# Performance work log

Hardware: AMD Instinct MI355X
Metric: run time of the kernel (lower is better)

## Reference

```python
import jax, jax.numpy as jnp
import numpy as np

NUM_EXPERTS = 64
TOP_K = 2
NOISE_STD = 1.0
LOAD_BALANCE_WEIGHT = 0.01
NOISE_KEY = jax.random.fold_in(jax.random.key(0), 12345)


def setup_inputs() -> dict:
    key = jax.random.key(0)
    k1, k2, k3 = jax.random.split(key, 3)
    B, S, D = 4, 4096, 1024
    x = jax.random.normal(k1, (B, S, D), dtype=jnp.float32)
    W_gate = jax.random.normal(k2, (NUM_EXPERTS, D), dtype=jnp.float32) * (1.0 / np.sqrt(D))
    W_noise = jax.random.normal(k3, (NUM_EXPERTS, D), dtype=jnp.float32) * (1.0 / np.sqrt(D))
    return {"x": x, "W_gate": W_gate, "W_noise": W_noise}


def reference(x, W_gate, W_noise):
    # x: [B,S,D], W_gate/W_noise: [E,D] (torch Linear weight layout)
    clean_logits = jnp.einsum("bsd,ed->bse", x, W_gate)           # [B,S,E]
    noise_scale = jax.nn.softplus(jnp.einsum("bsd,ed->bse", x, W_noise))
    noise = jax.random.normal(NOISE_KEY, clean_logits.shape, clean_logits.dtype)
    logits = clean_logits + noise * noise_scale * NOISE_STD

    probs = jax.nn.softmax(logits, axis=-1)                        # [B,S,E]
    routing_weights, expert_indices = jax.lax.top_k(probs, TOP_K)  # [B,S,K]
    routing_weights = routing_weights / jnp.sum(routing_weights, axis=-1, keepdims=True)

    # Load-balance loss on clean logits
    B, S, E = clean_logits.shape
    num_tokens = B * S
    expert_mask = jax.nn.one_hot(expert_indices, E, dtype=jnp.float32).sum(axis=2)  # [B,S,E]
    tokens_per_expert = expert_mask.sum(axis=(0, 1))               # [E]
    fraction_tokens = tokens_per_expert / num_tokens
    router_probs = jax.nn.softmax(clean_logits, axis=-1)
    mean_router_prob = router_probs.mean(axis=(0, 1))              # [E]
    load_balance_loss = LOAD_BALANCE_WEIGHT * E * jnp.sum(fraction_tokens * mean_router_prob)

    noise_scale_mean = noise_scale.mean()
    return (routing_weights, expert_indices, load_balance_loss, router_probs, noise_scale_mean)
```

## Files before the change

### kernel.cpp

```cpp
#include <hip/hip_runtime.h>
#include <stdint.h>

#define TOKENS 16384
#define DDIM   1024
#define NEXP   64
#define NCOL   128
#define TB     32
#define NBLK   (TOKENS / TB)
#define NCH    (DDIM / 32)
#define NTILE  8
#define CPP    4

typedef __attribute__((ext_vector_type(8))) short bf16x8;
typedef __attribute__((ext_vector_type(4))) float f32x4;

__device__ ushort g_wf[3][NTILE][NCH][64][8];
__device__ float g_ps[NEXP];
__device__ float g_cnt[NEXP];
__device__ float g_spa[1];

__device__ inline ushort bf16rne(float f) {
  uint32_t u = __float_as_uint(f);
  return (ushort)((u + 0x7fffu + ((u >> 16) & 1u)) >> 16);
}
__device__ inline float bf16tof(ushort h) {
  return __uint_as_float(((uint32_t)h) << 16);
}
__device__ inline void split3(float v, ushort& h, ushort& m, ushort& l) {
  h = bf16rne(v);
  float r1 = v - bf16tof(h);
  m = bf16rne(r1);
  float r2 = r1 - bf16tof(m);
  l = bf16rne(r2);
}

struct U2 { uint32_t a, b; };

__host__ __device__ constexpr U2 tf2x32(uint32_t k0, uint32_t k1,
                                        uint32_t x0, uint32_t x1) {
  uint32_t ks[3] = {k0, k1, k0 ^ k1 ^ 0x1BD11BDAu};
  const uint32_t rot[2][4] = {{13u, 15u, 26u, 6u}, {17u, 29u, 16u, 24u}};
  x0 += ks[0]; x1 += ks[1];
  for (int d = 0; d < 5; ++d) {
    for (int j = 0; j < 4; ++j) {
      uint32_t r = rot[d & 1][j];
      x0 += x1;
      x1 = (x1 << r) | (x1 >> (32u - r));
      x1 ^= x0;
    }
    x0 += ks[(d + 1) % 3];
    x1 += ks[(d + 2) % 3] + (uint32_t)(d + 1);
  }
  return U2{x0, x1};
}

__device__ inline uint32_t noise_bits(uint32_t i) {
  constexpr U2 NK = tf2x32(0u, 0u, 0u, 12345u);
  U2 o = tf2x32(NK.a, NK.b, 0u, i);
  return o.a ^ o.b;
}

__device__ inline float xla_erfinv(float x) {
  float w = -log1pf(-x * x);
  float p;
  if (w < 5.0f) {
    w = w - 2.5f;
    p = 2.81022636e-08f;
    p = 3.43273939e-07f + p * w;
    p = -3.5233877e-06f + p * w;
    p = -4.39150654e-06f + p * w;
    p = 0.00021858087f + p * w;
    p = -0.00125372503f + p * w;
    p = -0.00417768164f + p * w;
    p = 0.246640727f + p * w;
    p = 1.50140941f + p * w;
  } else {
    w = sqrtf(w) - 3.0f;
    p = -0.000200214257f;
    p = 0.000100950558f + p * w;
    p = 0.00134934322f + p * w;
    p = -0.00367342844f + p * w;
    p = 0.00573950773f + p * w;
    p = -0.0076224613f + p * w;
    p = 0.00943887047f + p * w;
    p = 1.00167406f + p * w;
    p = 2.83297682f + p * w;
  }
  return p * x;
}

__device__ inline float noise_normal(uint32_t i) {
  uint32_t bits = noise_bits(i);
  float f = __uint_as_float((bits >> 9) | 0x3f800000u) - 1.0f;
  float u = f * 2.0f + (-0.99999994f);
  u = fmaxf(u, -0.99999994f);
  return 1.41421356237f * xla_erfinv(u);
}

__device__ inline float softplus_ref(float x) {
  return fmaxf(x, 0.0f) + log1pf(expf(-fabsf(x)));
}

__device__ inline float wave_max64(float v) {
  #pragma unroll
  for (int off = 32; off; off >>= 1) v = fmaxf(v, __shfl_xor(v, off, 64));
  return v;
}
__device__ inline float wave_sum64(float v) {
  #pragma unroll
  for (int off = 32; off; off >>= 1) v += __shfl_xor(v, off, 64);
  return v;
}
__device__ inline void wave_argmax64(float v, int idx, float& mv, int& mi) {
  float bv = v; int bi = idx;
  #pragma unroll
  for (int off = 32; off; off >>= 1) {
    float ov = __shfl_xor(bv, off, 64);
    int   oi = __shfl_xor(bi, off, 64);
    if (ov > bv || (ov == bv && oi < bi)) { bv = ov; bi = oi; }
  }
  mv = bv; mi = bi;
}

__global__ __launch_bounds__(64)
void wsplit_kernel(const float* __restrict__ wg, const float* __restrict__ wn) {
  const int ct   = blockIdx.x >> 5;
  const int kc   = blockIdx.x & 31;
  const int lane = threadIdx.x;
  const int col  = ct * 16 + (lane & 15);
  const int koff = kc * 32 + (lane >> 4) * 8;
  const float* src = (col < NEXP) ? (wg + (size_t)col * DDIM)
                                  : (wn + (size_t)(col - NEXP) * DDIM);
  const float4 v0 = *(const float4*)&src[koff];
  const float4 v1 = *(const float4*)&src[koff + 4];
  const float av[8] = {v0.x, v0.y, v0.z, v0.w, v1.x, v1.y, v1.z, v1.w};
  union BF8 { bf16x8 v; ushort u[8]; };
  BF8 H, M, L;
  #pragma unroll
  for (int j = 0; j < 8; ++j) {
    ushort h, m, l;
    split3(av[j], h, m, l);
    H.u[j] = h; M.u[j] = m; L.u[j] = l;
  }
  *(bf16x8*)&g_wf[0][ct][kc][lane][0] = H.v;
  *(bf16x8*)&g_wf[1][ct][kc][lane][0] = M.v;
  *(bf16x8*)&g_wf[2][ct][kc][lane][0] = L.v;

  if (blockIdx.x == 0) {
    g_ps[lane] = 0.0f; g_cnt[lane] = 0.0f;
    if (lane == 0) g_spa[0] = 0.0f;
  }
}

__global__ __launch_bounds__(512, 8)
void NoisyTopKRouter_57621281243491_kernel(
    const float* __restrict__ x, float* __restrict__ out) {
  __shared__ ushort ldsA[3][2][CPP][64][8];

  const int tid  = threadIdx.x;
  const int w    = tid >> 6;
  const int lane = tid & 63;
  const int tok0 = blockIdx.x * TB;

  char* LA = (char*)&ldsA[0][0][0][0][0];

  const int srow = tid >> 4;
  const int skq  = tid & 15;
  const int stg  = srow >> 4;
  const int sfr  = srow & 15;
  const int sc   = skq >> 2;
  const int ss   = skq & 3;
  const int so   = (sc * 1024 + ss * 256 + sfr * 16) ^ ((skq & 7) << 4);
  const float* sx = x + (size_t)(tok0 + srow) * DDIM + skq * 8;

  const int fr_row = lane & 15;
  const int fr_s   = lane >> 4;
  const ushort* wf = &g_wf[0][0][0][0][0];
  const int b0 = w * 16384 + lane * 8;
  #define PS 131072

  f32x4 acc0 = {0.f, 0.f, 0.f, 0.f};
  f32x4 acc1 = {0.f, 0.f, 0.f, 0.f};

  float4 xa0, xa1, xb0, xb1;

  #define SPLIT_PHASE(X0, X1)                                             \
    {                                                                     \
      union BF8 { bf16x8 v; ushort u[8]; };                               \
      BF8 H, M, L;                                                        \
      const float av_[8] = {X0.x, X0.y, X0.z, X0.w, X1.x, X1.y, X1.z, X1.w}; \
      _Pragma("unroll")                                                   \
      for (int j = 0; j < 8; ++j) {                                       \
        ushort h_, m_, l_;                                                \
        split3(av_[j], h_, m_, l_);                                       \
        H.u[j] = h_; M.u[j] = m_; L.u[j] = l_;                            \
      }                                                                   \
      *(bf16x8*)(LA + stg * 4096 + so)         = H.v;                     \
      *(bf16x8*)(LA + 8192 + stg * 4096 + so)  = M.v;                     \
      *(bf16x8*)(LA + 16384 + stg * 4096 + so) = L.v;                     \
    }

  #define MFMA_PHASE(ph)                                                  \
    _Pragma("unroll")                                                     \
    for (int c = 0; c < CPP; ++c) {                                       \
      int ro = c * 1024 + lane * 16;                                      \
      ro ^= ((ro >> 8) & 7) << 4;                                         \
      const bf16x8 Ah0 = *(const bf16x8*)(LA + ro);                       \
      const bf16x8 Am0 = *(const bf16x8*)(LA + 8192 + ro);                \
      const bf16x8 Al0 = *(const bf16x8*)(LA + 16384 + ro);               \
      const bf16x8 Ah1 = *(const bf16x8*)(LA + 4096 + ro);                \
      const bf16x8 Am1 = *(const bf16x8*)(LA + 12288 + ro);               \
      const bf16x8 Al1 = *(const bf16x8*)(LA + 20480 + ro);               \
      const int co = ((ph) * CPP + c) * 512;                              \
      const bf16x8 Bh = *(const bf16x8*)&wf[b0 + co];                     \
      const bf16x8 Bm = *(const bf16x8*)&wf[b0 + PS + co];                \
      const bf16x8 Bl = *(const bf16x8*)&wf[b0 + 2 * PS + co];            \
      acc0 = __builtin_amdgcn_mfma_f32_16x16x32_bf16(Ah0, Bh, acc0, 0, 0, 0); \
      acc0 = __builtin_amdgcn_mfma_f32_16x16x32_bf16(Ah0, Bm, acc0, 0, 0, 0); \
      acc0 = __builtin_amdgcn_mfma_f32_16x16x32_bf16(Am0, Bh, acc0, 0, 0, 0); \
      acc0 = __builtin_amdgcn_mfma_f32_16x16x32_bf16(Ah0, Bl, acc0, 0, 0, 0); \
      acc0 = __builtin_amdgcn_mfma_f32_16x16x32_bf16(Al0, Bh, acc0, 0, 0, 0); \
      acc0 = __builtin_amdgcn_mfma_f32_16x16x32_bf16(Am0, Bm, acc0, 0, 0, 0); \
      acc1 = __builtin_amdgcn_mfma_f32_16x16x32_bf16(Ah1, Bh, acc1, 0, 0, 0); \
      acc1 = __builtin_amdgcn_mfma_f32_16x16x32_bf16(Ah1, Bm, acc1, 0, 0, 0); \
      acc1 = __builtin_amdgcn_mfma_f32_16x16x32_bf16(Am1, Bh, acc1, 0, 0, 0); \
      acc1 = __builtin_amdgcn_mfma_f32_16x16x32_bf16(Ah1, Bl, acc1, 0, 0, 0); \
      acc1 = __builtin_amdgcn_mfma_f32_16x16x32_bf16(Al1, Bh, acc1, 0, 0, 0); \
      acc1 = __builtin_amdgcn_mfma_f32_16x16x32_bf16(Am1, Bm, acc1, 0, 0, 0); \
    }

  #define DO_PHASE(ph, C0, C1, N0, N1, PRE)                               \
    SPLIT_PHASE(C0, C1);                                                  \
    if (PRE) {                                                            \
      N0 = *(const float4*)&sx[(ph + 1) * 128];                           \
      N1 = *(const float4*)&sx[(ph + 1) * 128 + 4];                       \
    }                                                                     \
    __syncthreads();                                                      \
    MFMA_PHASE(ph);                                                       \
    __syncthreads();

  xa0 = *(const float4*)&sx[0];
  xa1 = *(const float4*)&sx[4];

  DO_PHASE(0, xa0, xa1, xb0, xb1, 1);
  DO_PHASE(1, xb0, xb1, xa0, xa1, 1);
  DO_PHASE(2, xa0, xa1, xb0, xb1, 1);
  DO_PHASE(3, xb0, xb1, xa0, xa1, 1);
  DO_PHASE(4, xa0, xa1, xb0, xb1, 1);
  DO_PHASE(5, xb0, xb1, xa0, xa1, 1);
  DO_PHASE(6, xa0, xa1, xb0, xb1, 1);
  DO_PHASE(7, xb0, xb1, xa0, xa1, 0);

  #undef DO_PHASE
  #undef SPLIT_PHASE
  #undef MFMA_PHASE
  #undef PS

  float (*lds_logits)[NCOL + 4] = (float (*)[NCOL + 4])LA;
  float (*lps)[NEXP] = (float (*)[NEXP])(LA + 16896);
  float (*lcb)[NEXP] = (float (*)[NEXP])(LA + 18944);
  float* lspw        = (float*)(LA + 20992);

  #pragma unroll
  for (int r = 0; r < 4; ++r) {
    lds_logits[4 * fr_s + r][w * 16 + fr_row]      = acc0[r];
    lds_logits[16 + 4 * fr_s + r][w * 16 + fr_row] = acc1[r];
  }
  __syncthreads();

  float* out_rw  = out;
  float* out_idx = out + 2 * TOKENS;
  float* out_rp  = out + 4 * TOKENS + 1;

  float ps_acc = 0.0f, sp_acc = 0.0f, c_acc = 0.0f;

  for (int it = 0; it < 4; ++it) {
    const int tl = w * 4 + it;
    const int t  = tok0 + tl;
    const float cl = lds_logits[tl][lane];
    const float nl = lds_logits[tl][NEXP + lane];

    const float m  = wave_max64(cl);
    const float v  = expf(cl - m);
    const float Z  = wave_sum64(v);
    const float rp = v / Z;
    out_rp[(size_t)t * NEXP + lane] = rp;
    ps_acc += rp;

    const float ns  = softplus_ref(nl);
    sp_acc += ns;
    const float noi = noise_normal((uint32_t)(t * NEXP + lane));
    const float lgn = __fadd_rn(cl, __fmul_rn(noi, ns));

    const float m2 = wave_max64(lgn);
    const float v2 = expf(lgn - m2);
    const float Z2 = wave_sum64(v2);
    const float p  = v2 / Z2;

    float p1; int i1;
    wave_argmax64(p, lane, p1, i1);
    const float pm = (lane == i1) ? -3.402823466e38f : p;
    float p2; int i2;
    wave_argmax64(pm, lane, p2, i2);

    c_acc += (float)((lane == i1) + (lane == i2));

    if (lane == 0) {
      const float s = p1 + p2;
      out_rw[t * 2 + 0]  = p1 / s;
      out_rw[t * 2 + 1]  = p2 / s;
      out_idx[t * 2 + 0] = (float)i1;
      out_idx[t * 2 + 1] = (float)i2;
    }
  }

  lps[w][lane] = ps_acc;
  lcb[w][lane] = c_acc;
  const float spw = wave_sum64(sp_acc);
  if (lane == 0) lspw[w] = spw;
  __syncthreads();
  if (tid < NEXP) {
    float a = 0.0f, b = 0.0f;
    #pragma unroll
    for (int j = 0; j < 8; ++j) { a += lps[j][tid]; b += lcb[j][tid]; }
    atomicAdd(&g_ps[tid],  a);
    atomicAdd(&g_cnt[tid], b);
  }
  if (tid == 0) {
    float s = 0.0f;
    #pragma unroll
    for (int j = 0; j < 8; ++j) s += lspw[j];
    atomicAdd(&g_spa[0], s);
  }
}

__global__ void finalize_kernel(float* __restrict__ out) {
  const int lane = threadIdx.x;
  float term = (g_cnt[lane] / (float)TOKENS) * (g_ps[lane] / (float)TOKENS);
  #pragma unroll
  for (int off = 32; off; off >>= 1) term += __shfl_xor(term, off, 64);
  if (lane == 0) {
    out[4 * TOKENS] = 0.64f * term;
    out[4 * TOKENS + 1 + TOKENS * NEXP] = g_spa[0] / (float)(TOKENS * NEXP);
  }
}

extern "C" void kernel_launch(void* const* d_in, const int* in_sizes, int n_in,
                              void* d_out, int out_size, void* d_ws, size_t ws_size,
                              hipStream_t stream) {
  const float* x  = (const float*)d_in[0];
  const float* wg = (const float*)d_in[1];
  const float* wn = (const float*)d_in[2];
  float* out = (float*)d_out;

  (void)d_ws; (void)ws_size; (void)in_sizes; (void)n_in; (void)out_size;

  wsplit_kernel<<<NTILE * NCH, 64, 0, stream>>>(wg, wn);
  NoisyTopKRouter_57621281243491_kernel<<<NBLK, 512, 0, stream>>>(x, out);
  finalize_kernel<<<1, 64, 0, stream>>>(out);
}
```

Baseline: 143.1 us.

## Use 1024-thread blocks with per-wave token-half split and wider K chunks

Doubles the block to 16 waves. Each wave now computes one 16x16 output tile (one token half for one column tile) instead of two, and each phase stages twice as many K columns, so only 4 phases and barriers are needed instead of 8. This halves the per-wave MFMA chain length and accumulator registers and raises parallelism per block. In exchange it doubles LDS per block and uses larger blocks, which may reduce occupancy, and each B fragment from global is now loaded by two waves.

Measured after the change: 144.7 us. No clear change (+1.1%).

```diff
diff --git a/kernel.cpp b/kernel.cpp
--- a/kernel.cpp
+++ b/kernel.cpp
@@ -9,7 +9,7 @@
 #define NBLK   (TOKENS / TB)
 #define NCH    (DDIM / 32)
 #define NTILE  8
-#define CPP    4
+#define CPP    8
 
 typedef __attribute__((ext_vector_type(8))) short bf16x8;
 typedef __attribute__((ext_vector_type(4))) float f32x4;
@@ -152,7 +152,7 @@
   }
 }
 
-__global__ __launch_bounds__(512, 8)
+__global__ __launch_bounds__(1024, 8)
 void NoisyTopKRouter_57621281243491_kernel(
     const float* __restrict__ x, float* __restrict__ out) {
   __shared__ ushort ldsA[3][2][CPP][64][8];
@@ -160,27 +160,29 @@
   const int tid  = threadIdx.x;
   const int w    = tid >> 6;
   const int lane = tid & 63;
+  const int tg   = w & 1;
+  const int ct   = w >> 1;
   const int tok0 = blockIdx.x * TB;
 
   char* LA = (char*)&ldsA[0][0][0][0][0];
 
-  const int srow = tid >> 4;
-  const int skq  = tid & 15;
+  const int srow = tid >> 5;
+  const int skq  = tid & 31;
   const int stg  = srow >> 4;
   const int sfr  = srow & 15;
   const int sc   = skq >> 2;
   const int ss   = skq & 3;
-  const int so   = (sc * 1024 + ss * 256 + sfr * 16) ^ ((skq & 7) << 4);
+  const int so   = (sc * 1024 + ss * 256 + sfr * 16) ^ ((skq & 15) << 4);
   const float* sx = x + (size_t)(tok0 + srow) * DDIM + skq * 8;
 
   const int fr_row = lane & 15;
   const int fr_s   = lane >> 4;
   const ushort* wf = &g_wf[0][0][0][0][0];
-  const int b0 = w * 16384 + lane * 8;
+  const int b0 = ct * 16384 + lane * 8;
   #define PS 131072
-
-  f32x4 acc0 = {0.f, 0.f, 0.f, 0.f};
-  f32x4 acc1 = {0.f, 0.f, 0.f, 0.f};
+  const int abase = tg * 8192;
+
+  f32x4 acc = {0.f, 0.f, 0.f, 0.f};
 
   float4 xa0, xa1, xb0, xb1;
 
@@ -195,45 +197,36 @@
         split3(av_[j], h_, m_, l_);                                       \
         H.u[j] = h_; M.u[j] = m_; L.u[j] = l_;                            \
       }                                                                   \
-      *(bf16x8*)(LA + stg * 4096 + so)         = H.v;                     \
-      *(bf16x8*)(LA + 8192 + stg * 4096 + so)  = M.v;                     \
-      *(bf16x8*)(LA + 16384 + stg * 4096 + so) = L.v;                     \
+      *(bf16x8*)(LA + stg * 8192 + so)         = H.v;                     \
+      *(bf16x8*)(LA + 16384 + stg * 8192 + so) = M.v;                     \
+      *(bf16x8*)(LA + 32768 + stg * 8192 + so) = L.v;                     \
     }
 
   #define MFMA_PHASE(ph)                                                  \
     _Pragma("unroll")                                                     \
     for (int c = 0; c < CPP; ++c) {                                       \
       int ro = c * 1024 + lane * 16;                                      \
-      ro ^= ((ro >> 8) & 7) << 4;                                         \
-      const bf16x8 Ah0 = *(const bf16x8*)(LA + ro);                       \
-      const bf16x8 Am0 = *(const bf16x8*)(LA + 8192 + ro);                \
-      const bf16x8 Al0 = *(const bf16x8*)(LA + 16384 + ro);               \
-      const bf16x8 Ah1 = *(const bf16x8*)(LA + 4096 + ro);                \
-      const bf16x8 Am1 = *(const bf16x8*)(LA + 12288 + ro);               \
-      const bf16x8 Al1 = *(const bf16x8*)(LA + 20480 + ro);               \
+      ro ^= ((ro >> 8) & 15) << 4;                                        \
+      const bf16x8 Ah = *(const bf16x8*)(LA + abase + ro);                \
+      const bf16x8 Am = *(const bf16x8*)(LA + 16384 + abase + ro);        \
+      const bf16x8 Al = *(const bf16x8*)(LA + 32768 + abase + ro);        \
       const int co = ((ph) * CPP + c) * 512;                              \
       const bf16x8 Bh = *(const bf16x8*)&wf[b0 + co];                     \
       const bf16x8 Bm = *(const bf16x8*)&wf[b0 + PS + co];                \
       const bf16x8 Bl = *(const bf16x8*)&wf[b0 + 2 * PS + co];            \
-      acc0 = __builtin_amdgcn_mfma_f32_16x16x32_bf16(Ah0, Bh, acc0, 0, 0, 0); \
-      acc0 = __builtin_amdgcn_mfma_f32_16x16x32_bf16(Ah0, Bm, acc0, 0, 0, 0); \
-      acc0 = __builtin_amdgcn_mfma_f32_16x16x32_bf16(Am0, Bh, acc0, 0, 0, 0); \
-      acc0 = __builtin_amdgcn_mfma_f32_16x16x32_bf16(Ah0, Bl, acc0, 0, 0, 0); \
-      acc0 = __builtin_amdgcn_mfma_f32_16x16x32_bf16(Al0, Bh, acc0, 0, 0, 0); \
-      acc0 = __builtin_amdgcn_mfma_f32_16x16x32_bf16(Am0, Bm, acc0, 0, 0, 0); \
-      acc1 = __builtin_amdgcn_mfma_f32_16x16x32_bf16(Ah1, Bh, acc1, 0, 0, 0); \
-      acc1 = __builtin_amdgcn_mfma_f32_16x16x32_bf16(Ah1, Bm, acc1, 0, 0, 0); \
-      acc1 = __builtin_amdgcn_mfma_f32_16x16x32_bf16(Am1, Bh, acc1, 0, 0, 0); \
-      acc1 = __builtin_amdgcn_mfma_f32_16x16x32_bf16(Ah1, Bl, acc1, 0, 0, 0); \
-      acc1 = __builtin_amdgcn_mfma_f32_16x16x32_bf16(Al1, Bh, acc1, 0, 0, 0); \
-      acc1 = __builtin_amdgcn_mfma_f32_16x16x32_bf16(Am1, Bm, acc1, 0, 0, 0); \
+      acc = __builtin_amdgcn_mfma_f32_16x16x32_bf16(Ah, Bh, acc, 0, 0, 0); \
+      acc = __builtin_amdgcn_mfma_f32_16x16x32_bf16(Ah, Bm, acc, 0, 0, 0); \
+      acc = __builtin_amdgcn_mfma_f32_16x16x32_bf16(Am, Bh, acc, 0, 0, 0); \
+      acc = __builtin_amdgcn_mfma_f32_16x16x32_bf16(Ah, Bl, acc, 0, 0, 0); \
+      acc = __builtin_amdgcn_mfma_f32_16x16x32_bf16(Al, Bh, acc, 0, 0, 0); \
+      acc = __builtin_amdgcn_mfma_f32_16x16x32_bf16(Am, Bm, acc, 0, 0, 0); \
     }
 
   #define DO_PHASE(ph, C0, C1, N0, N1, PRE)                               \
     SPLIT_PHASE(C0, C1);                                                  \
     if (PRE) {                                                            \
-      N0 = *(const float4*)&sx[(ph + 1) * 128];                           \
-      N1 = *(const float4*)&sx[(ph + 1) * 128 + 4];                       \
+      N0 = *(const float4*)&sx[(ph + 1) * 256];                           \
+      N1 = *(const float4*)&sx[(ph + 1) * 256 + 4];                       \
     }                                                                     \
     __syncthreads();                                                      \
     MFMA_PHASE(ph);                                                       \
@@ -245,11 +238,7 @@
   DO_PHASE(0, xa0, xa1, xb0, xb1, 1);
   DO_PHASE(1, xb0, xb1, xa0, xa1, 1);
   DO_PHASE(2, xa0, xa1, xb0, xb1, 1);
-  DO_PHASE(3, xb0, xb1, xa0, xa1, 1);
-  DO_PHASE(4, xa0, xa1, xb0, xb1, 1);
-  DO_PHASE(5, xb0, xb1, xa0, xa1, 1);
-  DO_PHASE(6, xa0, xa1, xb0, xb1, 1);
-  DO_PHASE(7, xb0, xb1, xa0, xa1, 0);
+  DO_PHASE(3, xb0, xb1, xa0, xa1, 0);
 
   #undef DO_PHASE
   #undef SPLIT_PHASE
@@ -258,14 +247,12 @@
 
   float (*lds_logits)[NCOL + 4] = (float (*)[NCOL + 4])LA;
   float (*lps)[NEXP] = (float (*)[NEXP])(LA + 16896);
-  float (*lcb)[NEXP] = (float (*)[NEXP])(LA + 18944);
-  float* lspw        = (float*)(LA + 20992);
-
-  #pragma unroll
-  for (int r = 0; r < 4; ++r) {
-    lds_logits[4 * fr_s + r][w * 16 + fr_row]      = acc0[r];
-    lds_logits[16 + 4 * fr_s + r][w * 16 + fr_row] = acc1[r];
-  }
+  float (*lcb)[NEXP] = (float (*)[NEXP])(LA + 20992);
+  float* lspw        = (float*)(LA + 25088);
+
+  #pragma unroll
+  for (int r = 0; r < 4; ++r)
+    lds_logits[tg * 16 + 4 * fr_s + r][ct * 16 + fr_row] = acc[r];
   __syncthreads();
 
   float* out_rw  = out;
@@ -274,8 +261,8 @@
 
   float ps_acc = 0.0f, sp_acc = 0.0f, c_acc = 0.0f;
 
-  for (int it = 0; it < 4; ++it) {
-    const int tl = w * 4 + it;
+  for (int it = 0; it < 2; ++it) {
+    const int tl = w * 2 + it;
     const int t  = tok0 + tl;
     const float cl = lds_logits[tl][lane];
     const float nl = lds_logits[tl][NEXP + lane];
@@ -322,14 +309,14 @@
   if (tid < NEXP) {
     float a = 0.0f, b = 0.0f;
     #pragma unroll
-    for (int j = 0; j < 8; ++j) { a += lps[j][tid]; b += lcb[j][tid]; }
+    for (int j = 0; j < 16; ++j) { a += lps[j][tid]; b += lcb[j][tid]; }
     atomicAdd(&g_ps[tid],  a);
     atomicAdd(&g_cnt[tid], b);
   }
   if (tid == 0) {
     float s = 0.0f;
     #pragma unroll
-    for (int j = 0; j < 8; ++j) s += lspw[j];
+    for (int j = 0; j < 16; ++j) s += lspw[j];
     atomicAdd(&g_spa[0], s);
   }
 }
@@ -356,6 +343,6 @@
   (void)d_ws; (void)ws_size; (void)in_sizes; (void)n_in; (void)out_size;
 
   wsplit_kernel<<<NTILE * NCH, 64, 0, stream>>>(wg, wn);
-  NoisyTopKRouter_57621281243491_kernel<<<NBLK, 512, 0, stream>>>(x, out);
+  NoisyTopKRouter_57621281243491_kernel<<<NBLK, 1024, 0, stream>>>(x, out);
   finalize_kernel<<<1, 64, 0, stream>>>(out);
 }
```
